# Kernel tuning notes

Measured on AMD Instinct MI355X. Metric: run time of the kernel, lower is better.

Reference implementation:

```python
import jax, jax.numpy as jnp
import numpy as np

CODEBOOK_SIZE = 4096
EMBED_DIM = 256
BETA = 0.25


def setup_inputs() -> dict:
    key = jax.random.key(0)
    k_z, k_cb = jax.random.split(key)
    z = jax.random.normal(k_z, (32, 256, 32, 32), dtype=jnp.float32)
    # nn.Embedding weight init: uniform(-1/D, 1/D)
    codebook = jax.random.uniform(
        k_cb, (CODEBOOK_SIZE, EMBED_DIM), dtype=jnp.float32,
        minval=-1.0 / EMBED_DIM, maxval=1.0 / EMBED_DIM)
    return {"z": z, "codebook": codebook}


def reference(z, codebook):
    b, c, h, w = z.shape
    # (B,C,H,W) -> (B*H*W, D)
    z_flat = jnp.transpose(z, (0, 2, 3, 1)).reshape(-1, c)
    # squared euclidean distances: ||z||^2 - 2 z.e^T + ||e||^2  (== cdist(...)^2)
    z_sq = jnp.sum(z_flat * z_flat, axis=1, keepdims=True)          # (N,1)
    e_sq = jnp.sum(codebook * codebook, axis=1)                     # (K,)
    distances = z_sq - 2.0 * (z_flat @ codebook.T) + e_sq[None, :]  # (N,K)
    min_encoding_indices = jnp.argmin(distances, axis=1)            # (N,)
    z_q_flat = codebook[min_encoding_indices]                       # (N,D)
    z_q = jnp.transpose(z_q_flat.reshape(b, h, w, c), (0, 3, 1, 2))  # (B,C,H,W)
    # straight-through estimator
    z_q_st = z + jax.lax.stop_gradient(z_q - z)
    codebook_loss = jnp.mean((z_q - jax.lax.stop_gradient(z)) ** 2)
    commitment_loss = jnp.mean((z - jax.lax.stop_gradient(z_q)) ** 2)
    vq_loss = codebook_loss + BETA * commitment_loss
    return (z_q_st, vq_loss, min_encoding_indices.reshape(b, h, w))
```

## Files before the change

### kernel.cpp

```cpp
#include <hip/hip_runtime.h>

#define K_CODES 4096
#define D 256
#define N_VEC 32768
#define N_ELEM 8388608
#define WINDOW 3.5e-4f
#define RG 8
#define RSLICE 256

typedef _Float16 f16x8 __attribute__((ext_vector_type(8)));
typedef float f32x4 __attribute__((ext_vector_type(4)));

#define WS_LOSS 0
#define WS_COUNT 8
#define WS_DONE 16
#define WS_IDX 256
#define WS_LIST (WS_IDX + N_VEC * 4)
#define WS_ESQ (WS_LIST + N_VEC * 4)
#define WS_ZSQ (WS_ESQ + K_CODES * 4)
#define WS_APACK (WS_ZSQ + N_VEC * 4)
#define WS_BPACK (WS_APACK + (size_t)N_VEC * 256 * 2)
#define WS_RFIN (WS_BPACK + (size_t)K_CODES * 256 * 2 + 65536)

#define PREP_PZ 4096
#define PREP_PCB 512
#define PREP_ESQ 1024
#define PREP_ZSQ 128
#define PREP_BLOCKS (PREP_PZ + PREP_PCB + PREP_ESQ + PREP_ZSQ)

__device__ __forceinline__ unsigned long long pack_key(float s, int idx) {
  const unsigned u = __float_as_uint(s);
  const unsigned mk = (u & 0x80000000u) ? ~u : (u | 0x80000000u);
  return ((unsigned long long)mk << 12) | (unsigned long long)(unsigned)idx;
}
__device__ __forceinline__ float key_score(unsigned long long k) {
  const unsigned mk = (unsigned)(k >> 12);
  const unsigned u = (mk & 0x80000000u) ? (mk & 0x7fffffffu) : ~mk;
  return __uint_as_float(u);
}

__device__ __forceinline__ void pin_frag(f16x8& v) {
  asm volatile("" : "+v"(v));
}

__device__ void esq_body(int bx, const float* __restrict__ cb,
                         float* __restrict__ esq) {
  const int lane = threadIdx.x & 63;
  const int k = bx * 4 + (threadIdx.x >> 6);
  const float* row = cb + (size_t)k * D;
  double s = 0.;
#pragma unroll
  for (int j = 0; j < 4; ++j) {
    const float v = row[lane + 64 * j];
    s += (double)__fmul_rn(v, v);
  }
#pragma unroll
  for (int off = 32; off > 0; off >>= 1) s += __shfl_down(s, off, 64);
  if (lane == 0) esq[k] = (float)s;
}

__device__ void zsq_body(int bx, const float* __restrict__ z,
                         float* __restrict__ zsq) {
  const int n = bx * 256 + threadIdx.x;
  const int b = n >> 10;
  const int hw = n & 1023;
  const float* p = z + ((size_t)b << 18) + hw;
  double a0 = 0., a1 = 0., a2 = 0., a3 = 0.;
  for (int c = 0; c < D; c += 4) {
    const float v0 = p[(size_t)(c + 0) << 10];
    const float v1 = p[(size_t)(c + 1) << 10];
    const float v2 = p[(size_t)(c + 2) << 10];
    const float v3 = p[(size_t)(c + 3) << 10];
    a0 += (double)__fmul_rn(v0, v0);
    a1 += (double)__fmul_rn(v1, v1);
    a2 += (double)__fmul_rn(v2, v2);
    a3 += (double)__fmul_rn(v3, v3);
  }
  zsq[n] = (float)((a0 + a1) + (a2 + a3));
}

__device__ void pack_z2_body(int bx, const float* __restrict__ z,
                             _Float16* __restrict__ Ap) {
  const int t = bx * 256 + threadIdx.x;
  const int lane = t & 63;
  const int fid = t >> 6;
  const int ks = fid & 7;
  const int grp = fid >> 3;
  const int n = grp * 16 + (lane & 15);
  const int d = ks * 32 + ((lane >> 4) << 3);
  const int b = n >> 10, hw = n & 1023;
  const float* p = z + ((size_t)b << 18) + ((size_t)d << 10) + hw;
  f16x8 H;
#pragma unroll
  for (int j = 0; j < 8; ++j) H[j] = (_Float16)p[(size_t)j << 10];
  *(f16x8*)(Ap + (size_t)t * 8) = H;
}

__device__ void pack_cb2_body(int bx, const float* __restrict__ cb,
                              _Float16* __restrict__ Bp) {
  const int t = bx * 256 + threadIdx.x;
  const int lane = t & 63;
  const int fid = t >> 6;
  const int ks = fid & 7;
  const int grp = fid >> 3;
  const int k = grp * 16 + (lane & 15);
  const int d = ks * 32 + ((lane >> 4) << 3);
  const float* p = cb + (size_t)k * D + d;
  f16x8 H;
#pragma unroll
  for (int j = 0; j < 8; ++j) H[j] = (_Float16)(p[j] * 256.f);
  *(f16x8*)(Bp + (size_t)t * 8) = H;
}

__global__ __launch_bounds__(256) void prep_kernel(const float* __restrict__ z,
                                                   const float* __restrict__ cb,
                                                   float* __restrict__ esq,
                                                   float* __restrict__ zsq,
                                                   _Float16* __restrict__ Ap,
                                                   _Float16* __restrict__ Bp) {
  const int b = blockIdx.x;
  if (b < PREP_PZ) {
    pack_z2_body(b, z, Ap);
  } else if (b < PREP_PZ + PREP_PCB) {
    pack_cb2_body(b - PREP_PZ, cb, Bp);
  } else if (b < PREP_PZ + PREP_PCB + PREP_ESQ) {
    esq_body(b - PREP_PZ - PREP_PCB, cb, esq);
  } else {
    zsq_body(b - PREP_PZ - PREP_PCB - PREP_ESQ, z, zsq);
  }
}

#define CLUSTER(ACC, SN)                                                     \
  {                                                                          \
    __builtin_amdgcn_s_setprio(1);                                           \
    _Pragma("unroll") for (int ks = 0; ks < 8; ++ks) {                       \
      ACC[0] = __builtin_amdgcn_mfma_f32_16x16x32_f16(                       \
          b[ks], a[0][ks], ks ? ACC[0] : z4, 0, 0, 0);                       \
      ACC[1] = __builtin_amdgcn_mfma_f32_16x16x32_f16(                       \
          b[ks], a[1][ks], ks ? ACC[1] : z4, 0, 0, 0);                       \
      ACC[2] = __builtin_amdgcn_mfma_f32_16x16x32_f16(                       \
          b[ks], a[2][ks], ks ? ACC[2] : z4, 0, 0, 0);                       \
      ACC[3] = __builtin_amdgcn_mfma_f32_16x16x32_f16(                       \
          b[ks], a[3][ks], ks ? ACC[3] : z4, 0, 0, 0);                       \
      b[ks] = *(const f16x8*)(bbase + (size_t)(SN)*16384 + ks * 512);        \
    }                                                                        \
    __builtin_amdgcn_s_setprio(0);                                           \
  }

#define FOLD(ACC, S, EV)                                                     \
  {                                                                          \
    const int cb0 = (S)*64 + crow;                                           \
    const float ev[4] = {(EV).x, (EV).y, (EV).z, (EV).w};                    \
    _Pragma("unroll") for (int r = 0; r < 4; ++r) {                          \
      const int code = cb0 + r;                                              \
      _Pragma("unroll") for (int ni = 0; ni < 4; ++ni) {                     \
        const float s = fmaf(ACC[ni][r], -0.0078125f, ev[r]);                \
        s2[ni] = fminf(fmaxf(s, s1[ni]), s2[ni]);                            \
        if (s < s1[ni]) i1[ni] = code;                                       \
        s1[ni] = fminf(s1[ni], s);                                           \
      }                                                                      \
    }                                                                        \
  }

__global__ __launch_bounds__(512, 2) void dist2_kernel(
    const _Float16* __restrict__ Ap, const _Float16* __restrict__ Bp,
    const float* __restrict__ esq, int* __restrict__ idx,
    int* __restrict__ list, unsigned int* __restrict__ count,
    unsigned long long* __restrict__ rfin) {
  __shared__ unsigned long long mb[128][4][2];
  const int tid = threadIdx.x;
  const int lane = tid & 63;
  const int w = tid >> 6;
  const int wn = w >> 2;
  const int wc = w & 3;
  const int n0 = blockIdx.x * 128;

  f16x8 a[4][8];
  {
    const _Float16* ab =
        Ap + (size_t)((n0 + wn * 64) >> 4) * 4096 + (size_t)lane * 8;
#pragma unroll
    for (int ni = 0; ni < 4; ++ni)
#pragma unroll
      for (int ks = 0; ks < 8; ++ks) {
        a[ni][ks] = *(const f16x8*)(ab + (size_t)(ni * 8 + ks) * 512);
        pin_frag(a[ni][ks]);
      }
  }

  float s1[4], s2[4];
  int i1[4];
#pragma unroll
  for (int ni = 0; ni < 4; ++ni) {
    s1[ni] = 3.4e38f;
    s2[ni] = 3.4e38f;
    i1[ni] = 0;
  }

  const _Float16* bbase = Bp + (size_t)wc * 4096 + (size_t)lane * 8;
  const int crow = wc * 16 + ((lane >> 4) << 2);
  const f32x4 z4 = (f32x4)0.f;

  f16x8 b[8];
  f32x4 accA[4], accB[4];
#pragma unroll
  for (int ks = 0; ks < 8; ++ks)
    b[ks] = *(const f16x8*)(bbase + (size_t)ks * 512);
  float4 evA = *(const float4*)(esq + crow);

  CLUSTER(accA, 1)
  float4 evB = *(const float4*)(esq + 64 + crow);

  for (int s = 1; s < 63; s += 2) {
    CLUSTER(accB, s + 1)
    FOLD(accA, s - 1, evA)
    evA = *(const float4*)(esq + (s + 1) * 64 + crow);
    CLUSTER(accA, s + 2)
    FOLD(accB, s, evB)
    evB = *(const float4*)(esq + (s + 2) * 64 + crow);
  }
  CLUSTER(accB, 64)
  FOLD(accA, 62, evA)
  FOLD(accB, 63, evB)

  unsigned long long k1[4], k2[4];
#pragma unroll
  for (int ni = 0; ni < 4; ++ni) {
    float a1 = s1[ni], a2 = s2[ni];
    int ai1 = i1[ni];
#pragma unroll
    for (int m = 16; m <= 32; m <<= 1) {
      const float bv1 = __shfl_xor(a1, m, 64);
      const int bi1 = __shfl_xor(ai1, m, 64);
      const float bv2 = __shfl_xor(a2, m, 64);
      const float hi = fmaxf(a1, bv1);
      const bool take = (bv1 < a1) || (bv1 == a1 && bi1 < ai1);
      if (take) ai1 = bi1;
      a1 = fminf(a1, bv1);
      a2 = fminf(fminf(a2, bv2), hi);
    }
    k1[ni] = pack_key(a1, ai1);
    k2[ni] = pack_key(a2, 0);
  }
  if (lane < 16) {
#pragma unroll
    for (int ni = 0; ni < 4; ++ni) {
      const int nl = wn * 64 + ni * 16 + lane;
      mb[nl][wc][0] = k1[ni];
      mb[nl][wc][1] = k2[ni];
    }
  }
  __syncthreads();
  if (tid < 128) {
    unsigned long long m1 = ~0ull, m2 = ~0ull;
#pragma unroll
    for (int s = 0; s < 4; ++s) {
      const unsigned long long c1 = mb[tid][s][0];
      const unsigned long long c2 = mb[tid][s][1];
      if (c1 < m1) {
        m2 = m1;
        m1 = c1;
      } else if (c1 < m2) {
        m2 = c1;
      }
      if (c2 < m2) m2 = c2;
    }
    const int n = n0 + tid;
    idx[n] = (int)(m1 & 0xFFFULL);
    const bool flag = key_score(m2) - key_score(m1) < WINDOW;
    rfin[n] = flag ? ~0ull : 0ull;
    if (flag) {
      const unsigned pos = atomicAdd(count, 1u);
      if (pos < N_VEC) list[pos] = n;
    }
  }
}

__global__ __launch_bounds__(256) void rescan_kernel(
    const float* __restrict__ z, const float* __restrict__ cb,
    const float* __restrict__ esq, const float* __restrict__ zsq,
    const int* __restrict__ list, const unsigned int* __restrict__ count,
    unsigned long long* __restrict__ rfin) {
  __shared__ double zrow[RG][D];
  __shared__ int nloc[RG];
  __shared__ float zsv[RG];
  const int tid = threadIdx.x;
  const int lane = tid & 63;
  unsigned int cnt = *count;
  if (cnt > N_VEC) cnt = N_VEC;
  const unsigned G = (cnt + RG - 1) / RG;
  const unsigned nitems = G * (K_CODES / RSLICE);
  for (unsigned item = blockIdx.x; item < nitems; item += gridDim.x) {
    const unsigned g = item >> 4;
    const int s = item & 15;
    __syncthreads();
    if (tid < RG) {
      const unsigned r = g * RG + tid;
      const int n = (r < cnt) ? list[r] : list[cnt - 1];
      nloc[tid] = n;
      zsv[tid] = zsq[n];
    }
    __syncthreads();
    for (int i = tid; i < RG * D; i += 256) {
      const int p = i >> 8, c = i & 255;
      const int n = nloc[p];
      const int b = n >> 10, hw = n & 1023;
      zrow[p][c] = (double)z[((size_t)b << 18) + ((size_t)c << 10) + hw];
    }
    __syncthreads();
    const int k = s * RSLICE + tid;
    const float* row = cb + (size_t)k * D;
    double acc[RG];
#pragma unroll
    for (int p = 0; p < RG; ++p) acc[p] = 0.;
    for (int c = 0; c < D; c += 4) {
      const float4 r4 = *(const float4*)(row + c);
      const double rx = (double)r4.x, ry = (double)r4.y;
      const double rz = (double)r4.z, rw = (double)r4.w;
#pragma unroll
      for (int p = 0; p < RG; ++p) {
        const double2 za = *(const double2*)&zrow[p][c];
        const double2 zb = *(const double2*)&zrow[p][c + 2];
        double a = acc[p];
        a = fma(za.x, rx, a);
        a = fma(za.y, ry, a);
        a = fma(zb.x, rz, a);
        a = fma(zb.y, rw, a);
        acc[p] = a;
      }
    }
    const float ek = esq[k];
    unsigned long long best[RG];
#pragma unroll
    for (int p = 0; p < RG; ++p) {
      const float dotf = (float)acc[p];
      const float d = __fadd_rn(__fsub_rn(zsv[p], __fmul_rn(2.0f, dotf)), ek);
      best[p] = pack_key(d, k);
    }
#pragma unroll
    for (int p = 0; p < RG; ++p) {
#pragma unroll
      for (int off = 32; off > 0; off >>= 1)
        best[p] = min(best[p], __shfl_down(best[p], off, 64));
    }
    if (lane == 0) {
#pragma unroll
      for (int p = 0; p < RG; ++p) atomicMin(rfin + nloc[p], best[p]);
    }
  }
}

__global__ __launch_bounds__(256) void gather_kernel(
    const float* __restrict__ z, const float* __restrict__ cb,
    const int* __restrict__ idxarr, const unsigned long long* __restrict__ rfin,
    float* __restrict__ out, float* __restrict__ loss_acc,
    unsigned int* __restrict__ done) {
  const int tid = threadIdx.x;
  const int n0 = blockIdx.x * 64;
  const int hwl = tid & 63;
  const int c0 = tid >> 6;
  const int n = n0 + hwl;
  const int b = n >> 10;
  const int hw = n & 1023;
  const unsigned long long rf = rfin[n];
  const int idx = rf ? (int)(rf & 0xFFFULL) : idxarr[n];
  if (tid < 64) out[(size_t)N_ELEM + 1 + n] = (float)idx;
  const float* crow = cb + (size_t)idx * D;
  const size_t obase = ((size_t)b << 18) + hw;
  float part = 0.f;
#pragma unroll
  for (int c = c0; c < D; c += 4) {
    const float v = crow[c];
    const size_t o = obase + ((size_t)c << 10);
    const float diff = v - z[o];
    out[o] = v;
    part = fmaf(diff, diff, part);
  }
#pragma unroll
  for (int off = 32; off > 0; off >>= 1) part += __shfl_down(part, off, 64);
  __shared__ float red[4];
  if ((tid & 63) == 0) red[tid >> 6] = part;
  __syncthreads();
  if (tid == 0) {
    atomicAdd(loss_acc, red[0] + red[1] + red[2] + red[3]);
    __threadfence();
    const unsigned old = atomicAdd(done, 1u);
    if (old == gridDim.x - 1) {
      const float total = atomicAdd(loss_acc, 0.0f);
      out[N_ELEM] = 1.25f * total * (1.0f / (float)N_ELEM);
    }
  }
}

extern "C" void kernel_launch(void* const* d_in, const int* in_sizes, int n_in,
                              void* d_out, int out_size, void* d_ws,
                              size_t ws_size, hipStream_t stream) {
  const float* z = (const float*)d_in[0];
  const float* cb = (const float*)d_in[1];
  float* out = (float*)d_out;
  char* ws = (char*)d_ws;
  float* loss_acc = (float*)(ws + WS_LOSS);
  unsigned int* count = (unsigned int*)(ws + WS_COUNT);
  unsigned int* done = (unsigned int*)(ws + WS_DONE);
  int* idx = (int*)(ws + WS_IDX);
  int* list = (int*)(ws + WS_LIST);
  float* esq = (float*)(ws + WS_ESQ);
  float* zsq = (float*)(ws + WS_ZSQ);
  _Float16* Ap = (_Float16*)(ws + WS_APACK);
  _Float16* Bp = (_Float16*)(ws + WS_BPACK);
  unsigned long long* rfin = (unsigned long long*)(ws + WS_RFIN);

  hipMemsetAsync(ws, 0, 256, stream);
  prep_kernel<<<PREP_BLOCKS, 256, 0, stream>>>(z, cb, esq, zsq, Ap, Bp);
  dist2_kernel<<<N_VEC / 128, 512, 0, stream>>>(Ap, Bp, esq, idx, list, count,
                                                rfin);
  rescan_kernel<<<2048, 256, 0, stream>>>(z, cb, esq, zsq, list, count, rfin);
  gather_kernel<<<N_VEC / 64, 256, 0, stream>>>(z, cb, idx, rfin, out,
                                                loss_acc, done);
}
```

Measured before the change: 286.0 us.

## Collect near-min candidate codes during MFMA pass and rescan only those in fp64

During the fp16 distance pass each row now appends codebook indices whose score falls within a window of the running minimum to a per-row candidate list, capped at 128 entries. A new wave-per-row kernel recomputes exact fp64 distances only for those candidates, and the full 4096-code fp64 rescan runs only for rows whose list overflowed. The prep kernel also writes a row-major fp32 copy of z so the rescans read it contiguously. This adds atomics and branches inside the inner fold loop of the GEMM kernel, plus extra workspace writes, in exchange for a much smaller exact-rescan workload.

```diff
diff --git a/kernel.cpp b/kernel.cpp
--- a/kernel.cpp
+++ b/kernel.cpp
@@ -5,6 +5,8 @@
 #define N_VEC 32768
 #define N_ELEM 8388608
 #define WINDOW 3.5e-4f
+#define W_APPEND 4.0e-4f
+#define CMAX 128
 #define RG 8
 #define RSLICE 256
 
@@ -14,6 +16,7 @@
 #define WS_LOSS 0
 #define WS_COUNT 8
 #define WS_DONE 16
+#define WS_COUNT2 24
 #define WS_IDX 256
 #define WS_LIST (WS_IDX + N_VEC * 4)
 #define WS_ESQ (WS_LIST + N_VEC * 4)
@@ -21,6 +24,12 @@
 #define WS_APACK (WS_ZSQ + N_VEC * 4)
 #define WS_BPACK (WS_APACK + (size_t)N_VEC * 256 * 2)
 #define WS_RFIN (WS_BPACK + (size_t)K_CODES * 256 * 2 + 65536)
+#define WS_ZT (WS_RFIN + (size_t)N_VEC * 8)
+#define WS_NEED_ZT (WS_ZT + (size_t)N_VEC * D * 4)
+#define WS_CNT WS_NEED_ZT
+#define WS_CANDL (WS_CNT + (size_t)N_VEC * 4)
+#define WS_LISTB (WS_CANDL + (size_t)N_VEC * CMAX * 2)
+#define WS_NEED_CAND (WS_LISTB + (size_t)N_VEC * 4)
 
 #define PREP_PZ 4096
 #define PREP_PCB 512
@@ -80,7 +89,8 @@
 }
 
 __device__ void pack_z2_body(int bx, const float* __restrict__ z,
-                             _Float16* __restrict__ Ap) {
+                             _Float16* __restrict__ Ap,
+                             float* __restrict__ zT) {
   const int t = bx * 256 + threadIdx.x;
   const int lane = t & 63;
   const int fid = t >> 6;
@@ -90,10 +100,19 @@
   const int d = ks * 32 + ((lane >> 4) << 3);
   const int b = n >> 10, hw = n & 1023;
   const float* p = z + ((size_t)b << 18) + ((size_t)d << 10) + hw;
+  float v[8];
   f16x8 H;
 #pragma unroll
-  for (int j = 0; j < 8; ++j) H[j] = (_Float16)p[(size_t)j << 10];
+  for (int j = 0; j < 8; ++j) {
+    v[j] = p[(size_t)j << 10];
+    H[j] = (_Float16)v[j];
+  }
   *(f16x8*)(Ap + (size_t)t * 8) = H;
+  if (zT) {
+    float4* o = (float4*)(zT + (size_t)n * D + d);
+    o[0] = make_float4(v[0], v[1], v[2], v[3]);
+    o[1] = make_float4(v[4], v[5], v[6], v[7]);
+  }
 }
 
 __device__ void pack_cb2_body(int bx, const float* __restrict__ cb,
@@ -112,15 +131,14 @@
   *(f16x8*)(Bp + (size_t)t * 8) = H;
 }
 
-__global__ __launch_bounds__(256) void prep_kernel(const float* __restrict__ z,
-                                                   const float* __restrict__ cb,
-                                                   float* __restrict__ esq,
-                                                   float* __restrict__ zsq,
-                                                   _Float16* __restrict__ Ap,
-                                                   _Float16* __restrict__ Bp) {
+__global__ __launch_bounds__(256) void prep_kernel(
+    const float* __restrict__ z, const float* __restrict__ cb,
+    float* __restrict__ esq, float* __restrict__ zsq,
+    _Float16* __restrict__ Ap, _Float16* __restrict__ Bp,
+    float* __restrict__ zT) {
   const int b = blockIdx.x;
   if (b < PREP_PZ) {
-    pack_z2_body(b, z, Ap);
+    pack_z2_body(b, z, Ap, zT);
   } else if (b < PREP_PZ + PREP_PCB) {
     pack_cb2_body(b - PREP_PZ, cb, Bp);
   } else if (b < PREP_PZ + PREP_PCB + PREP_ESQ) {
@@ -155,18 +173,33 @@
       const int code = cb0 + r;                                              \
       _Pragma("unroll") for (int ni = 0; ni < 4; ++ni) {                     \
         const float s = fmaf(ACC[ni][r], -0.0078125f, ev[r]);                \
+        if (candl) {                                                         \
+          if (s < fminf(thr[ni], s1[ni]) + W_APPEND) {                       \
+            const unsigned pp = atomicAdd(&cnt[npos[ni]], 1u);               \
+            if (pp < CMAX)                                                   \
+              candl[(size_t)npos[ni] * CMAX + pp] = (unsigned short)code;    \
+          }                                                                  \
+        }                                                                    \
         s2[ni] = fminf(fmaxf(s, s1[ni]), s2[ni]);                            \
         if (s < s1[ni]) i1[ni] = code;                                       \
         s1[ni] = fminf(s1[ni], s);                                           \
       }                                                                      \
     }                                                                        \
+    if (candl) {                                                             \
+      _Pragma("unroll") for (int ni = 0; ni < 4; ++ni) {                     \
+        const float m_ = fminf(s1[ni], __shfl_xor(s1[ni], 16, 64));          \
+        thr[ni] = fminf(m_, __shfl_xor(m_, 32, 64));                         \
+      }                                                                      \
+    }                                                                        \
   }
 
 __global__ __launch_bounds__(512, 2) void dist2_kernel(
     const _Float16* __restrict__ Ap, const _Float16* __restrict__ Bp,
     const float* __restrict__ esq, int* __restrict__ idx,
     int* __restrict__ list, unsigned int* __restrict__ count,
-    unsigned long long* __restrict__ rfin) {
+    unsigned long long* __restrict__ rfin, unsigned int* __restrict__ cnt,
+    unsigned short* __restrict__ candl, int* __restrict__ listB,
+    unsigned int* __restrict__ count2) {
   __shared__ unsigned long long mb[128][4][2];
   const int tid = threadIdx.x;
   const int lane = tid & 63;
@@ -188,13 +221,15 @@
       }
   }
 
-  float s1[4], s2[4];
-  int i1[4];
+  float s1[4], s2[4], thr[4];
+  int i1[4], npos[4];
 #pragma unroll
   for (int ni = 0; ni < 4; ++ni) {
     s1[ni] = 3.4e38f;
     s2[ni] = 3.4e38f;
+    thr[ni] = 3.4e38f;
     i1[ni] = 0;
+    npos[ni] = n0 + wn * 64 + ni * 16 + (lane & 15);
   }
 
   const _Float16* bbase = Bp + (size_t)wc * 4096 + (size_t)lane * 8;
@@ -270,16 +305,76 @@
     const bool flag = key_score(m2) - key_score(m1) < WINDOW;
     rfin[n] = flag ? ~0ull : 0ull;
     if (flag) {
-      const unsigned pos = atomicAdd(count, 1u);
-      if (pos < N_VEC) list[pos] = n;
-    }
-  }
-}
-
-__global__ __launch_bounds__(256) void rescan_kernel(
-    const float* __restrict__ z, const float* __restrict__ cb,
+      if (cnt) {
+        const unsigned pos = atomicAdd(count, 1u);
+        if (pos < N_VEC) list[pos] = n;
+      }
+      const bool toB = (cnt == nullptr) || (atomicAdd(&cnt[n], 0u) > CMAX);
+      if (toB) {
+        const unsigned p2 = atomicAdd(count2, 1u);
+        if (p2 < N_VEC) listB[p2] = n;
+      }
+    }
+  }
+}
+
+__global__ __launch_bounds__(256) void rescanB_kernel(
+    const float* __restrict__ zT, const float* __restrict__ cb,
     const float* __restrict__ esq, const float* __restrict__ zsq,
     const int* __restrict__ list, const unsigned int* __restrict__ count,
+    const unsigned int* __restrict__ cnt,
+    const unsigned short* __restrict__ candl,
+    unsigned long long* __restrict__ rfin) {
+  if (!candl) return;
+  const int lane = threadIdx.x & 63;
+  const int wv = blockIdx.x * 4 + (threadIdx.x >> 6);
+  unsigned int cN = *count;
+  if (cN > N_VEC) cN = N_VEC;
+  for (unsigned i = wv; i < cN; i += gridDim.x * 4) {
+    const int n = list[i];
+    const unsigned c = cnt[n];
+    if (c > CMAX) continue;
+    const unsigned j0 = min((unsigned)(2 * lane), c - 1);
+    const unsigned j1 = min((unsigned)(2 * lane + 1), c - 1);
+    const int k0 = candl[(size_t)n * CMAX + j0];
+    const int k1 = candl[(size_t)n * CMAX + j1];
+    const float* r0 = cb + (size_t)k0 * D;
+    const float* r1 = cb + (size_t)k1 * D;
+    const float* zr = zT + (size_t)n * D;
+    double a0 = 0., a1 = 0.;
+    for (int cc = 0; cc < D; cc += 4) {
+      const float4 zf = *(const float4*)(zr + cc);
+      const double zx = (double)zf.x, zy = (double)zf.y;
+      const double zz = (double)zf.z, zw = (double)zf.w;
+      const float4 f0 = *(const float4*)(r0 + cc);
+      const float4 f1 = *(const float4*)(r1 + cc);
+      a0 = fma(zx, (double)f0.x, a0);
+      a0 = fma(zy, (double)f0.y, a0);
+      a0 = fma(zz, (double)f0.z, a0);
+      a0 = fma(zw, (double)f0.w, a0);
+      a1 = fma(zx, (double)f1.x, a1);
+      a1 = fma(zy, (double)f1.y, a1);
+      a1 = fma(zz, (double)f1.z, a1);
+      a1 = fma(zw, (double)f1.w, a1);
+    }
+    const float zs = zsq[n];
+    const float d0 =
+        __fadd_rn(__fsub_rn(zs, __fmul_rn(2.0f, (float)a0)), esq[k0]);
+    const float d1 =
+        __fadd_rn(__fsub_rn(zs, __fmul_rn(2.0f, (float)a1)), esq[k1]);
+    unsigned long long best = min(pack_key(d0, k0), pack_key(d1, k1));
+#pragma unroll
+    for (int off = 32; off > 0; off >>= 1)
+      best = min(best, __shfl_down(best, off, 64));
+    if (lane == 0) atomicMin(rfin + n, best);
+  }
+}
+
+__global__ __launch_bounds__(256) void rescan_kernel(
+    const float* __restrict__ z, const float* __restrict__ zT,
+    const float* __restrict__ cb, const float* __restrict__ esq,
+    const float* __restrict__ zsq, const int* __restrict__ list,
+    const unsigned int* __restrict__ count,
     unsigned long long* __restrict__ rfin) {
   __shared__ double zrow[RG][D];
   __shared__ int nloc[RG];
@@ -301,11 +396,18 @@
       zsv[tid] = zsq[n];
     }
     __syncthreads();
-    for (int i = tid; i < RG * D; i += 256) {
-      const int p = i >> 8, c = i & 255;
-      const int n = nloc[p];
-      const int b = n >> 10, hw = n & 1023;
-      zrow[p][c] = (double)z[((size_t)b << 18) + ((size_t)c << 10) + hw];
+    if (zT) {
+      for (int i = tid; i < RG * D; i += 256) {
+        const int p = i >> 8, c = i & 255;
+        zrow[p][c] = (double)zT[(size_t)nloc[p] * D + c];
+      }
+    } else {
+      for (int i = tid; i < RG * D; i += 256) {
+        const int p = i >> 8, c = i & 255;
+        const int n = nloc[p];
+        const int b = n >> 10, hw = n & 1023;
+        zrow[p][c] = (double)z[((size_t)b << 18) + ((size_t)c << 10) + hw];
+      }
     }
     __syncthreads();
     const int k = s * RSLICE + tid;
@@ -402,6 +504,7 @@
   float* loss_acc = (float*)(ws + WS_LOSS);
   unsigned int* count = (unsigned int*)(ws + WS_COUNT);
   unsigned int* done = (unsigned int*)(ws + WS_DONE);
+  unsigned int* count2 = (unsigned int*)(ws + WS_COUNT2);
   int* idx = (int*)(ws + WS_IDX);
   int* list = (int*)(ws + WS_LIST);
   float* esq = (float*)(ws + WS_ESQ);
@@ -409,12 +512,22 @@
   _Float16* Ap = (_Float16*)(ws + WS_APACK);
   _Float16* Bp = (_Float16*)(ws + WS_BPACK);
   unsigned long long* rfin = (unsigned long long*)(ws + WS_RFIN);
+  float* zT = (ws_size >= WS_NEED_ZT) ? (float*)(ws + WS_ZT) : nullptr;
+  const bool canduse = (ws_size >= WS_NEED_CAND) && (zT != nullptr);
+  unsigned int* cnt = canduse ? (unsigned int*)(ws + WS_CNT) : nullptr;
+  unsigned short* candl = canduse ? (unsigned short*)(ws + WS_CANDL) : nullptr;
+  int* listB = canduse ? (int*)(ws + WS_LISTB) : list;
 
   hipMemsetAsync(ws, 0, 256, stream);
-  prep_kernel<<<PREP_BLOCKS, 256, 0, stream>>>(z, cb, esq, zsq, Ap, Bp);
+  if (canduse) hipMemsetAsync(ws + WS_CNT, 0, (size_t)N_VEC * 4, stream);
+  prep_kernel<<<PREP_BLOCKS, 256, 0, stream>>>(z, cb, esq, zsq, Ap, Bp, zT);
   dist2_kernel<<<N_VEC / 128, 512, 0, stream>>>(Ap, Bp, esq, idx, list, count,
-                                                rfin);
-  rescan_kernel<<<2048, 256, 0, stream>>>(z, cb, esq, zsq, list, count, rfin);
+                                                rfin, cnt, candl, listB,
+                                                count2);
+  rescanB_kernel<<<512, 256, 0, stream>>>(zT, cb, esq, zsq, list, count, cnt,
+                                          candl, rfin);
+  rescan_kernel<<<2048, 256, 0, stream>>>(z, zT, cb, esq, zsq, listB, count2,
+                                          rfin);
   gather_kernel<<<N_VEC / 64, 256, 0, stream>>>(z, cb, idx, rfin, out,
                                                 loss_acc, done);
 }
```

Result: slower. 692.2 us (+142.0%).
